# Kernel tuning notes

Hardware: AMD Instinct MI355X
Metric: run time of the kernel (lower is better)

Reference implementation:

```python
import jax, jax.numpy as jnp
import numpy as np

D_MODEL = 1024
D_ATTN = 1024
BATCH = 4
SEQ = 2048


def setup_inputs() -> dict:
    key = jax.random.key(0)
    k_x, k_q, k_k, k_v = jax.random.split(key, 4)
    return {
        "x": jax.random.normal(k_x, (BATCH, SEQ, D_MODEL), dtype=jnp.float32),
        "Wq": jax.random.normal(k_q, (D_MODEL, D_ATTN), dtype=jnp.float32),
        "Wk": jax.random.normal(k_k, (D_MODEL, D_ATTN), dtype=jnp.float32),
        "Wv": jax.random.normal(k_v, (D_MODEL, D_ATTN), dtype=jnp.float32),
    }


def reference(x, Wq, Wk, Wv):
    # x: [B, S, D]; Wq/Wk/Wv: [D, Da]
    B, S, _ = x.shape
    Da = Wq.shape[1]
    Q = jnp.einsum("bsd,da->bsa", x, Wq)
    K = jnp.einsum("bsd,da->bsa", x, Wk)
    V = jnp.einsum("bsd,da->bsa", x, Wv)
    scores = jnp.einsum("bia,bja->bij", Q, K)  # [B, S, S]
    # Faithful to source: tril with diagonal=1 (allows attending one step ahead)
    i = jnp.arange(S)[:, None]
    j = jnp.arange(S)[None, :]
    allowed = j <= i + 1  # [S, S] bool
    scores = jnp.where(allowed[None, :, :], scores, -jnp.inf)
    scale = jnp.sqrt(jnp.asarray(Da, dtype=scores.dtype))
    attn = jax.nn.softmax(scores / scale, axis=-1)
    # dropout p=0 -> identity
    return jnp.einsum("bij,bja->bia", attn, V)
```

## Files before the change

### kernel.cpp

```cpp
#include <hip/hip_runtime.h>
#include <math.h>

#define BATCH 4
#define SEQ 2048
#define DM 1024
#define NTOK (BATCH * SEQ)
#define NE ((size_t)NTOK * DM)
#define WN ((size_t)DM * DM)

using s16x8 = __attribute__((ext_vector_type(8))) short;
using f32x4 = __attribute__((ext_vector_type(4))) float;

__device__ __forceinline__ unsigned short f2bf(float f) {
    unsigned u = __builtin_bit_cast(unsigned, f);
    u += 0x7FFFu + ((u >> 16) & 1u);
    return (unsigned short)(u >> 16);
}
__device__ __forceinline__ float bf2f(unsigned short h) {
    unsigned u = ((unsigned)h) << 16;
    return __builtin_bit_cast(float, u);
}

__device__ __forceinline__ f32x4 MFMA(s16x8 a, s16x8 b, f32x4 c) {
    return __builtin_amdgcn_mfma_f32_16x16x32_bf16(a, b, c, 0, 0, 0);
}

#define AS1 __attribute__((address_space(1)))
#define AS3 __attribute__((address_space(3)))
__device__ __forceinline__ void gll16(const void* g, void* l) {
    __builtin_amdgcn_global_load_lds((const AS1 void*)g, (AS3 void*)l, 16, 0, 0);
}

__device__ __forceinline__ s16x8 lds_frag(const short* base, int row, int g) {
    return *(const s16x8*)(base + row * 64 + ((g ^ (row & 7)) << 3));
}

__device__ __forceinline__ void stage_tile(const unsigned short* g0, size_t rs,
                                           short* lds, int tid) {
    int lane = tid & 63, w = tid >> 6;
    #pragma unroll
    for (int c = 0; c < 4; ++c) {
        int s = c * 256 + w * 64 + lane;
        int row = s >> 3, gg = s & 7;
        int graw = gg ^ (row & 7);
        gll16(g0 + (size_t)row * rs + graw * 8, lds + (size_t)s * 8);
    }
}

__global__ __launch_bounds__(256) void split_x(const float* __restrict__ x,
                                               unsigned short* __restrict__ xh,
                                               unsigned short* __restrict__ xl) {
    size_t n4 = NE / 4;
    for (size_t i = (size_t)blockIdx.x * 256 + threadIdx.x; i < n4;
         i += (size_t)gridDim.x * 256) {
        float4 v = ((const float4*)x)[i];
        ushort4 h, l;
        h.x = f2bf(v.x); l.x = f2bf(v.x - bf2f(h.x));
        h.y = f2bf(v.y); l.y = f2bf(v.y - bf2f(h.y));
        h.z = f2bf(v.z); l.z = f2bf(v.z - bf2f(h.z));
        h.w = f2bf(v.w); l.w = f2bf(v.w - bf2f(h.w));
        ((ushort4*)xh)[i] = h;
        ((ushort4*)xl)[i] = l;
    }
}

__global__ __launch_bounds__(256) void split_w(
    const float* __restrict__ Wq, const float* __restrict__ Wk,
    const float* __restrict__ Wv,
    unsigned short* __restrict__ Wqh, unsigned short* __restrict__ Wql,
    unsigned short* __restrict__ Wkh, unsigned short* __restrict__ Wkl,
    unsigned short* __restrict__ Wvt) {
    const int z = blockIdx.z;
    const int tid = threadIdx.x;
    if (z < 2) {
        const float* W = z ? Wk : Wq;
        unsigned short* oh = z ? Wkh : Wqh;
        unsigned short* ol = z ? Wkl : Wql;
        size_t n4 = WN / 4;
        size_t stride = (size_t)gridDim.x * gridDim.y * 256;
        for (size_t i = ((size_t)blockIdx.y * gridDim.x + blockIdx.x) * 256 + tid;
             i < n4; i += stride) {
            float4 v = ((const float4*)W)[i];
            ushort4 h, l;
            h.x = f2bf(v.x); l.x = f2bf(v.x - bf2f(h.x));
            h.y = f2bf(v.y); l.y = f2bf(v.y - bf2f(h.y));
            h.z = f2bf(v.z); l.z = f2bf(v.z - bf2f(h.z));
            h.w = f2bf(v.w); l.w = f2bf(v.w - bf2f(h.w));
            ((ushort4*)oh)[i] = h;
            ((ushort4*)ol)[i] = l;
        }
    } else {
        __shared__ float t[64][65];
        const int d0 = blockIdx.x * 64, n0 = blockIdx.y * 64;
        #pragma unroll
        for (int c = 0; c < 16; ++c) {
            int f = c * 256 + tid; int r = f >> 6, cc = f & 63;
            t[r][cc] = Wv[(size_t)(d0 + r) * DM + n0 + cc];
        }
        __syncthreads();
        #pragma unroll
        for (int c = 0; c < 16; ++c) {
            int f = c * 256 + tid; int r = f >> 6, cc = f & 63;
            Wvt[(size_t)(n0 + r) * DM + d0 + cc] = f2bf(t[cc][r]);
        }
    }
}

__global__ __launch_bounds__(256, 2) void mvt_fused(
    const unsigned short* __restrict__ Wkh_, const unsigned short* __restrict__ Wkl_,
    const unsigned short* __restrict__ Wqh_, const unsigned short* __restrict__ Wql_,
    float* __restrict__ Mslab,
    const unsigned short* __restrict__ Wvt_, const unsigned short* __restrict__ xh_,
    unsigned short* __restrict__ Vt) {
    __shared__ short L[4 * 128 * 64];
    short* Ah = L;            short* Al = L + 128 * 64;
    short* Bh = L + 2 * 128 * 64; short* Bl = L + 3 * 128 * 64;
    const int tid = threadIdx.x, lane = tid & 63, w = tid >> 6;
    const int wr = w >> 1, wc = w & 1;
    const int bid = blockIdx.x;

    f32x4 acc[4][4];
    #pragma unroll
    for (int i = 0; i < 4; ++i)
        #pragma unroll
        for (int j = 0; j < 4; ++j) acc[i][j] = (f32x4){0.f, 0.f, 0.f, 0.f};

    if (bid < 512) {
        const int kz = bid >> 6, rem = bid & 63;
        const int m0 = (rem & 7) * 128, n0 = (rem >> 3) * 128;
        #pragma unroll
        for (int kk = 0; kk < 2; ++kk) {
            const int k0 = kz * 128 + kk * 64;
            stage_tile(Wkh_ + (size_t)m0 * DM + k0, DM, Ah, tid);
            stage_tile(Wkl_ + (size_t)m0 * DM + k0, DM, Al, tid);
            stage_tile(Wqh_ + (size_t)n0 * DM + k0, DM, Bh, tid);
            stage_tile(Wql_ + (size_t)n0 * DM + k0, DM, Bl, tid);
            __syncthreads();
            #pragma unroll
            for (int ks = 0; ks < 2; ++ks) {
                const int g = ks * 4 + (lane >> 4);
                s16x8 a_h[4], a_l[4], b_h[4], b_l[4];
                #pragma unroll
                for (int mi = 0; mi < 4; ++mi) {
                    int r = wr * 64 + mi * 16 + (lane & 15);
                    a_h[mi] = lds_frag(Ah, r, g);
                    a_l[mi] = lds_frag(Al, r, g);
                }
                #pragma unroll
                for (int ni = 0; ni < 4; ++ni) {
                    int r = wc * 64 + ni * 16 + (lane & 15);
                    b_h[ni] = lds_frag(Bh, r, g);
                    b_l[ni] = lds_frag(Bl, r, g);
                }
                #pragma unroll
                for (int mi = 0; mi < 4; ++mi)
                    #pragma unroll
                    for (int ni = 0; ni < 4; ++ni) {
                        acc[mi][ni] = MFMA(a_h[mi], b_h[ni], acc[mi][ni]);
                        acc[mi][ni] = MFMA(a_h[mi], b_l[ni], acc[mi][ni]);
                        acc[mi][ni] = MFMA(a_l[mi], b_h[ni], acc[mi][ni]);
                    }
            }
            __syncthreads();
        }
        float* out = Mslab + (size_t)kz * WN;
        #pragma unroll
        for (int mi = 0; mi < 4; ++mi)
            #pragma unroll
            for (int ni = 0; ni < 4; ++ni)
                #pragma unroll
                for (int r = 0; r < 4; ++r) {
                    int row = m0 + wr * 64 + mi * 16 + (lane >> 4) * 4 + r;
                    int col = n0 + wc * 64 + ni * 16 + (lane & 15);
                    out[(size_t)row * DM + col] = acc[mi][ni][r];
                }
    } else {
        const int id2 = bid - 512;
        const int m0 = (id2 & 7) * 128;
        const int n0 = (id2 >> 3) * 128;
        for (int k0 = 0; k0 < DM; k0 += 64) {
            stage_tile(Wvt_ + (size_t)m0 * DM + k0, DM, Ah, tid);
            stage_tile(xh_ + (size_t)n0 * DM + k0, DM, Bh, tid);
            __syncthreads();
            #pragma unroll
            for (int ks = 0; ks < 2; ++ks) {
                const int g = ks * 4 + (lane >> 4);
                s16x8 a_h[4], b_h[4];
                #pragma unroll
                for (int mi = 0; mi < 4; ++mi)
                    a_h[mi] = lds_frag(Ah, wr * 64 + mi * 16 + (lane & 15), g);
                #pragma unroll
                for (int ni = 0; ni < 4; ++ni)
                    b_h[ni] = lds_frag(Bh, wc * 64 + ni * 16 + (lane & 15), g);
                #pragma unroll
                for (int mi = 0; mi < 4; ++mi)
                    #pragma unroll
                    for (int ni = 0; ni < 4; ++ni)
                        acc[mi][ni] = MFMA(a_h[mi], b_h[ni], acc[mi][ni]);
            }
            __syncthreads();
        }
        #pragma unroll
        for (int mi = 0; mi < 4; ++mi)
            #pragma unroll
            for (int ni = 0; ni < 4; ++ni)
                #pragma unroll
                for (int r = 0; r < 4; ++r) {
                    int row = m0 + wr * 64 + mi * 16 + (lane >> 4) * 4 + r;
                    int col = n0 + wc * 64 + ni * 16 + (lane & 15);
                    Vt[(size_t)row * NTOK + col] = f2bf(acc[mi][ni][r]);
                }
    }
}

__global__ __launch_bounds__(256) void mreduce(
    const float* __restrict__ Mslab,
    unsigned short* __restrict__ Mh, unsigned short* __restrict__ Ml) {
    size_t i = (size_t)blockIdx.x * 256 + threadIdx.x;
    float4 s = ((const float4*)Mslab)[i];
    #pragma unroll
    for (int r = 1; r < 8; ++r) {
        float4 v = ((const float4*)(Mslab + (size_t)r * WN))[i];
        s.x += v.x; s.y += v.y; s.z += v.z; s.w += v.w;
    }
    ushort4 h, l;
    h.x = f2bf(s.x); l.x = f2bf(s.x - bf2f(h.x));
    h.y = f2bf(s.y); l.y = f2bf(s.y - bf2f(h.y));
    h.z = f2bf(s.z); l.z = f2bf(s.z - bf2f(h.z));
    h.w = f2bf(s.w); l.w = f2bf(s.w - bf2f(h.w));
    ((ushort4*)Mh)[i] = h;
    ((ushort4*)Ml)[i] = l;
}

__global__ __launch_bounds__(256, 2) void gemm3_split(
    const unsigned short* __restrict__ Ah_, const unsigned short* __restrict__ Al_,
    const unsigned short* __restrict__ Bh_, const unsigned short* __restrict__ Bl_,
    unsigned short* __restrict__ Ch, unsigned short* __restrict__ Cl) {
    const int m0 = blockIdx.x * 128, n0 = blockIdx.y * 128;
    __shared__ short Ah[128 * 64], Al[128 * 64], Bh[128 * 64], Bl[128 * 64];
    const int tid = threadIdx.x, lane = tid & 63, w = tid >> 6;
    const int wr = w >> 1, wc = w & 1;

    f32x4 acc[4][4];
    #pragma unroll
    for (int i = 0; i < 4; ++i)
        #pragma unroll
        for (int j = 0; j < 4; ++j) acc[i][j] = (f32x4){0.f, 0.f, 0.f, 0.f};

    for (int k0 = 0; k0 < DM; k0 += 64) {
        stage_tile(Ah_ + (size_t)m0 * DM + k0, DM, Ah, tid);
        stage_tile(Al_ + (size_t)m0 * DM + k0, DM, Al, tid);
        stage_tile(Bh_ + (size_t)n0 * DM + k0, DM, Bh, tid);
        stage_tile(Bl_ + (size_t)n0 * DM + k0, DM, Bl, tid);
        __syncthreads();
        #pragma unroll
        for (int ks = 0; ks < 2; ++ks) {
            const int g = ks * 4 + (lane >> 4);
            s16x8 a_h[4], a_l[4], b_h[4], b_l[4];
            #pragma unroll
            for (int mi = 0; mi < 4; ++mi) {
                int r = wr * 64 + mi * 16 + (lane & 15);
                a_h[mi] = lds_frag(Ah, r, g);
                a_l[mi] = lds_frag(Al, r, g);
            }
            #pragma unroll
            for (int ni = 0; ni < 4; ++ni) {
                int r = wc * 64 + ni * 16 + (lane & 15);
                b_h[ni] = lds_frag(Bh, r, g);
                b_l[ni] = lds_frag(Bl, r, g);
            }
            #pragma unroll
            for (int mi = 0; mi < 4; ++mi)
                #pragma unroll
                for (int ni = 0; ni < 4; ++ni) {
                    acc[mi][ni] = MFMA(a_h[mi], b_h[ni], acc[mi][ni]);
                    acc[mi][ni] = MFMA(a_h[mi], b_l[ni], acc[mi][ni]);
                    acc[mi][ni] = MFMA(a_l[mi], b_h[ni], acc[mi][ni]);
                }
        }
        __syncthreads();
    }
    #pragma unroll
    for (int mi = 0; mi < 4; ++mi)
        #pragma unroll
        for (int ni = 0; ni < 4; ++ni)
            #pragma unroll
            for (int r = 0; r < 4; ++r) {
                int row = m0 + wr * 64 + mi * 16 + (lane >> 4) * 4 + r;
                int col = n0 + wc * 64 + ni * 16 + (lane & 15);
                float v = acc[mi][ni][r];
                unsigned short h = f2bf(v);
                size_t o = (size_t)row * DM + col;
                Ch[o] = h;
                Cl[o] = f2bf(v - bf2f(h));
            }
}

__global__ __launch_bounds__(256, 2) void scores_mfma(
    const unsigned short* __restrict__ Yh, const unsigned short* __restrict__ Yl,
    const unsigned short* __restrict__ xh, const unsigned short* __restrict__ xl,
    float* __restrict__ P) {
    const int lin = (blockIdx.z * gridDim.y + blockIdx.y) * gridDim.x + blockIdx.x;
    const int logical = (lin & 7) * 128 + (lin >> 3);
    const int jt = logical & 15, t = (logical >> 4) & 15, b = logical >> 8;
    if (jt > t + 1) return;
    const int m0 = t * 128, n0 = jt * 128;
    const size_t qrow0 = (size_t)b * SEQ + m0;
    const size_t krow0 = (size_t)b * SEQ + n0;

    __shared__ short Ah[128 * 64], Al[128 * 64], Bh[128 * 64], Bl[128 * 64];
    const int tid = threadIdx.x, lane = tid & 63, w = tid >> 6;
    const int wr = w >> 1, wc = w & 1;

    f32x4 acc[4][4];
    #pragma unroll
    for (int i = 0; i < 4; ++i)
        #pragma unroll
        for (int j = 0; j < 4; ++j) acc[i][j] = (f32x4){0.f, 0.f, 0.f, 0.f};

    for (int k0 = 0; k0 < DM; k0 += 64) {
        stage_tile(Yh + qrow0 * DM + k0, DM, Ah, tid);
        stage_tile(Yl + qrow0 * DM + k0, DM, Al, tid);
        stage_tile(xh + krow0 * DM + k0, DM, Bh, tid);
        stage_tile(xl + krow0 * DM + k0, DM, Bl, tid);
        __syncthreads();
        #pragma unroll
        for (int ks = 0; ks < 2; ++ks) {
            const int g = ks * 4 + (lane >> 4);
            s16x8 a_h[4], a_l[4], b_h[4], b_l[4];
            #pragma unroll
            for (int mi = 0; mi < 4; ++mi) {
                int r = wr * 64 + mi * 16 + (lane & 15);
                a_h[mi] = lds_frag(Ah, r, g);
                a_l[mi] = lds_frag(Al, r, g);
            }
            #pragma unroll
            for (int ni = 0; ni < 4; ++ni) {
                int r = wc * 64 + ni * 16 + (lane & 15);
                b_h[ni] = lds_frag(Bh, r, g);
                b_l[ni] = lds_frag(Bl, r, g);
            }
            #pragma unroll
            for (int mi = 0; mi < 4; ++mi)
                #pragma unroll
                for (int ni = 0; ni < 4; ++ni) {
                    acc[mi][ni] = MFMA(a_h[mi], b_h[ni], acc[mi][ni]);
                    acc[mi][ni] = MFMA(a_h[mi], b_l[ni], acc[mi][ni]);
                    acc[mi][ni] = MFMA(a_l[mi], b_h[ni], acc[mi][ni]);
                }
        }
        __syncthreads();
    }
    const float scale = 1.0f / 32.0f;
    #pragma unroll
    for (int mi = 0; mi < 4; ++mi)
        #pragma unroll
        for (int ni = 0; ni < 4; ++ni)
            #pragma unroll
            for (int r = 0; r < 4; ++r) {
                int i = m0 + wr * 64 + mi * 16 + (lane >> 4) * 4 + r;
                int j = n0 + wc * 64 + ni * 16 + (lane & 15);
                float v = (j <= i + 1) ? acc[mi][ni][r] * scale : -INFINITY;
                P[((size_t)b * SEQ + i) * SEQ + j] = v;
            }
}

__global__ __launch_bounds__(256) void softmax_bf16(
    const float* __restrict__ P, unsigned short* __restrict__ P2) {
    const int row = blockIdx.x;
    const int b = row >> 11, i = row & (SEQ - 1);
    const int t = i >> 7;
    const int L = min(SEQ, (t + 2) * 128);
    const float* p = P + ((size_t)b * SEQ + i) * SEQ;
    unsigned short* q = P2 + ((size_t)b * SEQ + i) * SEQ;
    const int tid = threadIdx.x;
    __shared__ float red[4];

    float v[8];
    #pragma unroll
    for (int c = 0; c < 8; ++c) {
        int j = c * 256 + tid;
        v[c] = (j < L) ? p[j] : -INFINITY;
    }
    float m = -INFINITY;
    #pragma unroll
    for (int c = 0; c < 8; ++c) m = fmaxf(m, v[c]);
    #pragma unroll
    for (int o = 32; o > 0; o >>= 1) m = fmaxf(m, __shfl_xor(m, o));
    if ((tid & 63) == 0) red[tid >> 6] = m;
    __syncthreads();
    m = fmaxf(fmaxf(red[0], red[1]), fmaxf(red[2], red[3]));
    __syncthreads();

    float s = 0.f;
    #pragma unroll
    for (int c = 0; c < 8; ++c) { v[c] = __expf(v[c] - m); s += v[c]; }
    #pragma unroll
    for (int o = 32; o > 0; o >>= 1) s += __shfl_xor(s, o);
    if ((tid & 63) == 0) red[tid >> 6] = s;
    __syncthreads();
    s = red[0] + red[1] + red[2] + red[3];
    const float inv = 1.f / s;

    #pragma unroll
    for (int c = 0; c < 8; ++c) {
        int j = c * 256 + tid;
        if (j < L) q[j] = f2bf(v[c] * inv);
    }
}

__global__ __launch_bounds__(256, 2) void pv_mfma(
    const unsigned short* __restrict__ P2, const unsigned short* __restrict__ Vt,
    float* __restrict__ Out) {
    const int lin = (blockIdx.z * gridDim.y + blockIdx.y) * gridDim.x + blockIdx.x;
    const int logical = (lin & 7) * 64 + (lin >> 3);
    const int bx = logical & 7, t = (logical >> 3) & 15, b = logical >> 7;
    const int m0 = t * 128, n0 = bx * 128;
    const int jlim = min(SEQ, (t + 2) * 128);

    __shared__ short Pa[128 * 64], Vb[128 * 64];
    const int tid = threadIdx.x, lane = tid & 63, w = tid >> 6;
    const int wr = w >> 1, wc = w & 1;

    f32x4 acc[4][4];
    #pragma unroll
    for (int i = 0; i < 4; ++i)
        #pragma unroll
        for (int j = 0; j < 4; ++j) acc[i][j] = (f32x4){0.f, 0.f, 0.f, 0.f};

    for (int k0 = 0; k0 < jlim; k0 += 64) {
        stage_tile(P2 + ((size_t)b * SEQ + m0) * SEQ + k0, SEQ, Pa, tid);
        stage_tile(Vt + (size_t)n0 * NTOK + (size_t)b * SEQ + k0, NTOK, Vb, tid);
        __syncthreads();
        #pragma unroll
        for (int ks = 0; ks < 2; ++ks) {
            const int g = ks * 4 + (lane >> 4);
            s16x8 a_h[4], b_h[4];
            #pragma unroll
            for (int mi = 0; mi < 4; ++mi)
                a_h[mi] = lds_frag(Pa, wr * 64 + mi * 16 + (lane & 15), g);
            #pragma unroll
            for (int ni = 0; ni < 4; ++ni)
                b_h[ni] = lds_frag(Vb, wc * 64 + ni * 16 + (lane & 15), g);
            #pragma unroll
            for (int mi = 0; mi < 4; ++mi)
                #pragma unroll
                for (int ni = 0; ni < 4; ++ni)
                    acc[mi][ni] = MFMA(a_h[mi], b_h[ni], acc[mi][ni]);
        }
        __syncthreads();
    }
    #pragma unroll
    for (int mi = 0; mi < 4; ++mi)
        #pragma unroll
        for (int ni = 0; ni < 4; ++ni)
            #pragma unroll
            for (int r = 0; r < 4; ++r) {
                int i = m0 + wr * 64 + mi * 16 + (lane >> 4) * 4 + r;
                int col = n0 + wc * 64 + ni * 16 + (lane & 15);
                Out[((size_t)b * SEQ + i) * DM + col] = acc[mi][ni][r];
            }
}

extern "C" void kernel_launch(void* const* d_in, const int* in_sizes, int n_in,
                              void* d_out, int out_size, void* d_ws, size_t ws_size,
                              hipStream_t stream) {
    const float* x  = (const float*)d_in[0];
    const float* Wq = (const float*)d_in[1];
    const float* Wk = (const float*)d_in[2];
    const float* Wv = (const float*)d_in[3];

    char* ws = (char*)d_ws;
    unsigned short* Vt = (unsigned short*)ws;
    unsigned short* xh = (unsigned short*)(ws + 2 * NE);
    unsigned short* xl = (unsigned short*)(ws + 4 * NE);
    float* P = (float*)(ws + 6 * NE);
    unsigned short* P2 = (unsigned short*)(ws + 2 * NE);
    unsigned short* Wqh = (unsigned short*)(ws + 6 * NE);
    unsigned short* Wql = Wqh + WN;
    unsigned short* Wkh = Wql + WN;
    unsigned short* Wkl = Wkh + WN;
    unsigned short* Mh  = Wkl + WN;
    unsigned short* Ml  = Mh + WN;
    unsigned short* Wvt = Ml + WN;
    float* Mslab = (float*)(ws + 6 * NE + 7 * WN * 2);
    unsigned short* Yh = (unsigned short*)d_out;
    unsigned short* Yl = Yh + NE;

    split_x<<<2048, 256, 0, stream>>>(x, xh, xl);
    {
        dim3 g(16, 16, 3);
        split_w<<<g, 256, 0, stream>>>(Wq, Wk, Wv, Wqh, Wql, Wkh, Wkl, Wvt);
    }
    mvt_fused<<<1024, 256, 0, stream>>>(Wkh, Wkl, Wqh, Wql, Mslab, Wvt, xh, Vt);
    mreduce<<<1024, 256, 0, stream>>>(Mslab, Mh, Ml);
    {
        dim3 g(NTOK / 128, DM / 128);
        gemm3_split<<<g, 256, 0, stream>>>(xh, xl, Mh, Ml, Yh, Yl);
    }
    {
        dim3 g(16, 16, 4);
        scores_mfma<<<g, 256, 0, stream>>>(Yh, Yl, xh, xl, P);
    }
    softmax_bf16<<<BATCH * SEQ, 256, 0, stream>>>(P, P2);
    {
        dim3 g(8, 16, 4);
        pv_mfma<<<g, 256, 0, stream>>>(P2, Vt, (float*)d_out);
    }
}
```

Baseline: 297.2 us.

## Compact causal score grid and special-case superdiagonal tiles with single dot

The scores kernel now launches only the needed lower-triangular-plus-one tiles (604 blocks) instead of a full 16x16x4 grid with early exits, and balances jobs across the eight XCDs. Tiles one step above the diagonal only need a single unmasked element, so they fill -inf and compute that one dot product with a small reduction instead of running a full MFMA tile. The Y GEMM also gets an XCD-aware block remap. This removes wasted blocks and about 64 full GEMM tiles, at the cost of a serial loop for job decoding and some tail imbalance.

```diff
diff --git a/kernel.cpp b/kernel.cpp
--- a/kernel.cpp
+++ b/kernel.cpp
@@ -236,7 +236,9 @@
     const unsigned short* __restrict__ Ah_, const unsigned short* __restrict__ Al_,
     const unsigned short* __restrict__ Bh_, const unsigned short* __restrict__ Bl_,
     unsigned short* __restrict__ Ch, unsigned short* __restrict__ Cl) {
-    const int m0 = blockIdx.x * 128, n0 = blockIdx.y * 128;
+    const int lin = blockIdx.x;
+    const int job = (lin & 7) * 64 + (lin >> 3);
+    const int m0 = (job >> 3) * 128, n0 = (job & 7) * 128;
     __shared__ short Ah[128 * 64], Al[128 * 64], Bh[128 * 64], Bl[128 * 64];
     const int tid = threadIdx.x, lane = tid & 63, w = tid >> 6;
     const int wr = w >> 1, wc = w & 1;
@@ -300,16 +302,53 @@
     const unsigned short* __restrict__ Yh, const unsigned short* __restrict__ Yl,
     const unsigned short* __restrict__ xh, const unsigned short* __restrict__ xl,
     float* __restrict__ P) {
-    const int lin = (blockIdx.z * gridDim.y + blockIdx.y) * gridDim.x + blockIdx.x;
-    const int logical = (lin & 7) * 128 + (lin >> 3);
-    const int jt = logical & 15, t = (logical >> 4) & 15, b = logical >> 8;
-    if (jt > t + 1) return;
+    const int lin = blockIdx.x;
+    const int xcd = lin & 7, o = lin >> 3;
+    const int job = (xcd < 4 ? xcd * 76 : 4 * 76 + (xcd - 4) * 75) + o;
+    const int b = job / 151;
+    int rem = job % 151;
+    int t = 0;
+    while (true) {
+        int c = (t + 2 > 16) ? 16 : t + 2;
+        if (rem < c) break;
+        rem -= c; ++t;
+    }
+    const int jt = rem;
     const int m0 = t * 128, n0 = jt * 128;
     const size_t qrow0 = (size_t)b * SEQ + m0;
     const size_t krow0 = (size_t)b * SEQ + n0;
+    const int tid = threadIdx.x;
+
+    if (jt == t + 1) {
+        #pragma unroll
+        for (int c = 0; c < 16; ++c) {
+            int f = c * 256 + tid;
+            int r = f >> 5, cc = f & 31;
+            *(float4*)(P + ((size_t)b * SEQ + m0 + r) * SEQ + n0 + cc * 4) =
+                (float4){-INFINITY, -INFINITY, -INFINITY, -INFINITY};
+        }
+        __syncthreads();
+        if (tid < 64) {
+            const size_t yrow = (qrow0 + 127) * DM;
+            const size_t xrow = krow0 * DM;
+            float s = 0.f;
+            #pragma unroll
+            for (int e = 0; e < 16; ++e) {
+                int d = tid * 16 + e;
+                float yhv = bf2f(Yh[yrow + d]), ylv = bf2f(Yl[yrow + d]);
+                float xhv = bf2f(xh[xrow + d]), xlv = bf2f(xl[xrow + d]);
+                s += yhv * xhv + yhv * xlv + ylv * xhv;
+            }
+            #pragma unroll
+            for (int o2 = 32; o2 > 0; o2 >>= 1) s += __shfl_xor(s, o2);
+            if (tid == 0)
+                P[((size_t)b * SEQ + m0 + 127) * SEQ + n0] = s * (1.0f / 32.0f);
+        }
+        return;
+    }
 
     __shared__ short Ah[128 * 64], Al[128 * 64], Bh[128 * 64], Bl[128 * 64];
-    const int tid = threadIdx.x, lane = tid & 63, w = tid >> 6;
+    const int lane = tid & 63, w = tid >> 6;
     const int wr = w >> 1, wc = w & 1;
 
     f32x4 acc[4][4];
@@ -494,14 +533,8 @@
     }
     mvt_fused<<<1024, 256, 0, stream>>>(Wkh, Wkl, Wqh, Wql, Mslab, Wvt, xh, Vt);
     mreduce<<<1024, 256, 0, stream>>>(Mslab, Mh, Ml);
-    {
-        dim3 g(NTOK / 128, DM / 128);
-        gemm3_split<<<g, 256, 0, stream>>>(xh, xl, Mh, Ml, Yh, Yl);
-    }
-    {
-        dim3 g(16, 16, 4);
-        scores_mfma<<<g, 256, 0, stream>>>(Yh, Yl, xh, xl, P);
-    }
+    gemm3_split<<<512, 256, 0, stream>>>(xh, xl, Mh, Ml, Yh, Yl);
+    scores_mfma<<<604, 256, 0, stream>>>(Yh, Yl, xh, xl, P);
     softmax_bf16<<<BATCH * SEQ, 256, 0, stream>>>(P, P2);
     {
         dim3 g(8, 16, 4);
```

Result: no change. 298.1 us (+0.3%).
